# Kernel optimization log

Measured on AMD Instinct MI355X. Metric: run time of the kernel, lower is better.

Reference implementation:

```python
import jax, jax.numpy as jnp
import numpy as np

B, S, D = 2, 2048, 1024
H = 16            # attention heads
KVH = 4           # key/value heads
G = H // KVH      # group_size = 4
HD = D // H       # head_dim = 64
ROPE_THETA = 10000.0


def rope(x):
    # x: [B, S, D]; interleaved-pair rotary embedding over full last dim
    d = x.shape[-1]
    inv_freq = 1.0 / (ROPE_THETA ** (jnp.arange(0, d, 2, dtype=jnp.float32) / d))  # [d/2]
    ang = jnp.arange(x.shape[1], dtype=jnp.float32)[:, None] * inv_freq[None, :]   # [S, d/2]
    cos, sin = jnp.cos(ang), jnp.sin(ang)
    x1, x2 = x[..., 0::2], x[..., 1::2]
    r1 = x1 * cos - x2 * sin
    r2 = x1 * sin + x2 * cos
    out = jnp.stack([r1, r2], axis=-1).reshape(x.shape)
    return out


def setup_inputs() -> dict:
    key = jax.random.key(0)
    kx, kq, kk, kv = jax.random.split(key, 4)
    x = jax.random.normal(kx, (B, S, D), dtype=jnp.float32)
    # mark last 256 positions of batch element 1 as padding via NaN
    x = x.at[1, S - 256:, :].set(jnp.nan)
    scale = 1.0 / np.sqrt(D)
    Wq = jax.random.normal(kq, (D, D), dtype=jnp.float32) * scale
    Wk = jax.random.normal(kk, (D, D // G), dtype=jnp.float32) * scale
    Wv = jax.random.normal(kv, (D, D // G), dtype=jnp.float32) * scale
    return {"x": x, "Wq": Wq, "Wk": Wk, "Wv": Wv}


def reference(x, Wq, Wk, Wv):
    pad = jnp.isnan(x)                      # [B,S,D]
    x = jnp.where(pad, 0.0, x)
    key_pad = jnp.any(pad, axis=-1)         # [B,S] True = padded token

    q = x @ Wq                              # [B,S,D]
    k = jnp.repeat(x @ Wk, G, axis=-1)      # grouped KV, repeat_interleave -> [B,S,D]
    v = jnp.repeat(x @ Wv, G, axis=-1)

    q = rope(q)
    k = rope(k)

    def split_heads(t):
        return t.reshape(B, S, H, HD).transpose(0, 2, 1, 3)  # [B,H,S,HD]

    q, k, v = split_heads(q), split_heads(k), split_heads(v)

    scores = jnp.einsum('bhqd,bhkd->bhqk', q, k) / np.sqrt(HD)
    causal = jnp.tril(jnp.ones((S, S), dtype=bool))
    allow = causal[None, None, :, :] & (~key_pad)[:, None, None, :]
    scores = jnp.where(allow, scores, -1e9)
    attn = jax.nn.softmax(scores, axis=-1)
    out = jnp.einsum('bhqk,bhkd->bhqd', attn, v)
    return out.transpose(0, 2, 1, 3).reshape(B, S, D)
```

## Files before the change

kernel.cpp:

```cpp
#include <hip/hip_runtime.h>
#include <hip/hip_bf16.h>
#include <math.h>

typedef unsigned short u16;
typedef unsigned int u32;
typedef __bf16 bf16x8 __attribute__((ext_vector_type(8)));
typedef float fx4 __attribute__((ext_vector_type(4)));

#define MFMA16(a, b, c) __builtin_amdgcn_mfma_f32_16x16x32_bf16(a, b, c, 0, 0, 0)

static constexpr int Bb = 2, Ss = 2048, Dd = 1024, Hh = 16, DKV = 256;
static constexpr int NQKV = 1536;
static constexpr int ROWS = Bb * Ss;
static constexpr float L2T_OVER = 0.0259525632f;
static constexpr float SC2 = 0.18033688f;
static constexpr int PSTR = 76;

__device__ __forceinline__ u16 f2bf(float f) {
    union { float f; u32 i; } v; v.f = f;
    u32 u = v.i;
    return (u16)((u + 0x7FFFu + ((u >> 16) & 1u)) >> 16);
}
__device__ __forceinline__ u16 bfr(float f) {
    return (u16)((__float_as_uint(f) + 0x8000u) >> 16);
}

__device__ __forceinline__ void gl16(const u16* g, u16* l) {
    __builtin_amdgcn_global_load_lds(
        (const __attribute__((address_space(1))) void*)g,
        (__attribute__((address_space(3))) void*)l, 16, 0, 0);
}

template <int CTRL>
__device__ __forceinline__ float dppf(float x) {
    return __int_as_float(
        __builtin_amdgcn_mov_dpp(__float_as_int(x), CTRL, 0xF, 0xF, true));
}
__device__ __forceinline__ float rsum16(float x) {
    x += dppf<0xB1>(x);
    x += dppf<0x4E>(x);
    x += dppf<0x124>(x);
    x += dppf<0x128>(x);
    return x;
}

__global__ void pre_kernel(const float* __restrict__ x, const float* __restrict__ Wq,
                           const float* __restrict__ Wk, const float* __restrict__ Wv,
                           u16* __restrict__ xc, u32* __restrict__ kpb,
                           u16* __restrict__ wAll) {
    __shared__ u16 tile[32][33];
    __shared__ int flag;
    int bid = blockIdx.x, t = threadIdx.x;
    if (bid < 4096) {
        int row = bid;
        if (t == 0) flag = 0;
        __syncthreads();
        float4 d = *(const float4*)(x + (size_t)row * Dd + t * 4);
        int any = 0;
        float a0 = d.x, a1 = d.y, a2 = d.z, a3 = d.w;
        if ((__float_as_uint(a0) & 0x7FFFFFFFu) > 0x7F800000u) { a0 = 0.f; any = 1; }
        if ((__float_as_uint(a1) & 0x7FFFFFFFu) > 0x7F800000u) { a1 = 0.f; any = 1; }
        if ((__float_as_uint(a2) & 0x7FFFFFFFu) > 0x7F800000u) { a2 = 0.f; any = 1; }
        if ((__float_as_uint(a3) & 0x7FFFFFFFu) > 0x7F800000u) { a3 = 0.f; any = 1; }
        if (any) atomicOr(&flag, 1);
        uint2 o;
        o.x = (u32)f2bf(a0) | ((u32)f2bf(a1) << 16);
        o.y = (u32)f2bf(a2) | ((u32)f2bf(a3) << 16);
        *(uint2*)(xc + (size_t)row * Dd + t * 4) = o;
        __syncthreads();
        if (t == 0 && flag) {
            int b = row >> 11, s = row & (Ss - 1);
            atomicOr(&kpb[b * 64 + (s >> 5)], 1u << (s & 31));
        }
        return;
    }
    const float* in; u16* out; int C, bx, by;
    if (bid < 5120) { int i = bid - 4096; in = Wq; out = wAll; C = Dd; bx = i & 31; by = i >> 5; }
    else if (bid < 5376) { int i = bid - 5120; in = Wk; out = wAll + (size_t)Dd * Dd; C = DKV; bx = i & 7; by = i >> 3; }
    else { int i = bid - 5376; in = Wv; out = wAll + (size_t)1280 * Dd; C = DKV; bx = i & 7; by = i >> 3; }
    int c0 = bx * 32, r0 = by * 32;
    int tx = t & 31, ty = t >> 5;
    for (int i = 0; i < 32; i += 8)
        tile[ty + i][tx] = f2bf(in[(size_t)(r0 + ty + i) * C + c0 + tx]);
    __syncthreads();
    for (int i = 0; i < 32; i += 8)
        out[(size_t)(c0 + ty + i) * Dd + r0 + tx] = tile[tx][ty + i];
}

__global__ __launch_bounds__(256) void gemm_qkv(
    const u16* __restrict__ A, const u16* __restrict__ Bt, u16* __restrict__ C) {
    __shared__ __align__(16) u16 As[2][128 * 32];
    __shared__ __align__(16) u16 Bs[2][128 * 32];
    int t = threadIdx.x, w = t >> 6, lane = t & 63;
    int l15 = lane & 15, quad = lane >> 4;
    int col0 = blockIdx.x * 128, row0 = blockIdx.y * 128;
    int wm = w >> 1, wn = w & 1;
    fx4 acc[4][4];
#pragma unroll
    for (int i = 0; i < 4; ++i)
#pragma unroll
        for (int j = 0; j < 4; ++j) acc[i][j] = (fx4){0.f, 0.f, 0.f, 0.f};

    auto stage = [&](int kb, int buf) {
#pragma unroll
        for (int i = 0; i < 2; ++i) {
            int slot = i * 256 + t;
            int row = slot >> 2, p = slot & 3, g = p ^ ((row >> 1) & 3);
            gl16(A + (size_t)(row0 + row) * Dd + kb * 32 + g * 8,
                 &As[buf][(i * 256 + w * 64) * 8]);
            gl16(Bt + (size_t)(col0 + row) * Dd + kb * 32 + g * 8,
                 &Bs[buf][(i * 256 + w * 64) * 8]);
        }
    };

    stage(0, 0);
    int buf = 0;
    for (int kb = 0; kb < 32; ++kb) {
        __syncthreads();
        if (kb + 1 < 32) stage(kb + 1, buf ^ 1);
        bf16x8 af[4], bfr4[4];
#pragma unroll
        for (int mi = 0; mi < 4; ++mi) {
            int row = wm * 64 + mi * 16 + l15;
            af[mi] = *(const bf16x8*)(&As[buf][row * 32 + ((quad ^ ((row >> 1) & 3)) * 8)]);
        }
#pragma unroll
        for (int ni = 0; ni < 4; ++ni) {
            int row = wn * 64 + ni * 16 + l15;
            bfr4[ni] = *(const bf16x8*)(&Bs[buf][row * 32 + ((quad ^ ((row >> 1) & 3)) * 8)]);
        }
#pragma unroll
        for (int mi = 0; mi < 4; ++mi)
#pragma unroll
            for (int ni = 0; ni < 4; ++ni)
                acc[mi][ni] = MFMA16(af[mi], bfr4[ni], acc[mi][ni]);
        buf ^= 1;
    }
#pragma unroll
    for (int mi = 0; mi < 4; ++mi) {
        int rbase = row0 + wm * 64 + mi * 16 + quad * 4;
#pragma unroll
        for (int ni = 0; ni < 4; ++ni) {
            int ccol = col0 + wn * 64 + ni * 16 + l15;
#pragma unroll
            for (int r = 0; r < 4; ++r)
                C[(size_t)(rbase + r) * NQKV + ccol] = f2bf(acc[mi][ni][r]);
        }
    }
}

__global__ void post_kernel(const u16* __restrict__ qkv, u16* __restrict__ kr,
                            u16* __restrict__ vtb) {
    __shared__ u16 tile[32][33];
    int bid = blockIdx.x, t = threadIdx.x;
    if (bid < 4096) {
        int row = bid;
        float pos = (float)(row & (Ss - 1));
        float kv = __uint_as_float(((u32)qkv[(size_t)row * NQKV + Dd + t]) << 16);
        float j0 = (float)(2 * t), j1 = j0 + 1.0f;
        float f0 = exp2f(-j0 * L2T_OVER), f1 = exp2f(-j1 * L2T_OVER);
        float s0, c0, s1, c1;
        sincosf(pos * f0, &s0, &c0);
        sincosf(pos * f1, &s1, &c1);
        float r0 = kv * (c0 - s0), r1 = kv * (s0 + c0);
        float r2 = kv * (c1 - s1), r3 = kv * (s1 + c1);
        uint2 o;
        o.x = (u32)f2bf(r0) | ((u32)f2bf(r1) << 16);
        o.y = (u32)f2bf(r2) | ((u32)f2bf(r3) << 16);
        *(uint2*)(kr + (size_t)row * Dd + t * 4) = o;
        return;
    }
    int i = bid - 4096;
    int b = i >> 9, by = (i & 511) >> 3, bx = i & 7;
    int c0 = bx * 32, r0 = by * 32;
    int tx = t & 31, ty = t >> 5;
    for (int k = 0; k < 32; k += 8)
        tile[ty + k][tx] = qkv[(size_t)(b * Ss + r0 + ty + k) * NQKV + 1280 + c0 + tx];
    __syncthreads();
    for (int k = 0; k < 32; k += 8)
        vtb[(size_t)(b * DKV + c0 + ty + k) * Ss + r0 + tx] = tile[tx][ty + k];
}

__device__ __forceinline__ bf16x8 ropeFrag(uint4 raw, float pos, float jbase) {
    u32 W[4] = {raw.x, raw.y, raw.z, raw.w};
    union { u32 u[4]; bf16x8 v; } o;
#pragma unroll
    for (int c = 0; c < 4; ++c) {
        float x0 = __uint_as_float(W[c] << 16);
        float x1 = __uint_as_float(W[c] & 0xFFFF0000u);
        float f = exp2f(-(jbase + (float)c) * L2T_OVER);
        float sn, cs;
        sincosf(pos * f, &sn, &cs);
        float r0 = x0 * cs - x1 * sn, r1 = x0 * sn + x1 * cs;
        o.u[c] = (u32)f2bf(r0) | ((u32)f2bf(r1) << 16);
    }
    return o.v;
}

__global__ __launch_bounds__(256) void attn_kernel(
    const u16* __restrict__ qkv, const u16* __restrict__ kr,
    const u16* __restrict__ vt, const u32* __restrict__ kpb,
    float* __restrict__ out) {
    __shared__ __align__(16) u16 Ks[2][64 * 64];
    __shared__ __align__(16) u16 Vs[2][16 * 64];
    __shared__ __align__(16) u16 Ps[4][16 * PSTR];

    int t = threadIdx.x, w = t >> 6, lane = t & 63;
    int l15 = lane & 15, quad = lane >> 4;
    int bid = blockIdx.x;
    int u = bid >> 5, g = u >> 3, i = u & 7;
    int tile = (g == 0) ? (31 - i) : (g == 1) ? (16 + i) : (g == 2) ? (15 - i) : i;
    int hh = bid & 31, b = hh >> 4, h = hh & 15;
    int q0 = tile * 64;
    int nkb = tile + 1;

    int pos = q0 + w * 16 + l15;
    const u16* qp = qkv + (size_t)(b * Ss + pos) * NQKV + h * 64;
    float jb = (float)(h * 32 + quad * 4);
    bf16x8 qf0 = ropeFrag(*(const uint4*)(qp + quad * 8), (float)pos, jb);
    bf16x8 qf1 = ropeFrag(*(const uint4*)(qp + 32 + quad * 8), (float)pos, jb + 16.f);

    auto stageK = [&](int k0, int buf) {
#pragma unroll
        for (int i2 = 0; i2 < 2; ++i2) {
            int row = i2 * 32 + w * 8 + (lane >> 3);
            int gg = (lane & 7) ^ (row & 7);
            gl16(kr + (size_t)(b * Ss + k0 + row) * Dd + h * 64 + gg * 8,
                 &Ks[buf][(i2 * 32 + w * 8) * 64]);
        }
    };
    auto stageV = [&](int k0, int buf) {
        if (w < 2) {
            int row = w * 8 + (lane >> 3);
            int gg = (lane & 7) ^ (row & 7);
            gl16(vt + (size_t)(b * DKV + h * 16 + row) * Ss + k0 + gg * 8,
                 &Vs[buf][(w * 8) * 64]);
        }
    };

    float l_lane[4] = {0.f, 0.f, 0.f, 0.f};
    fx4 oacc = (fx4){0.f, 0.f, 0.f, 0.f};

    stageK(0, 0);
    stageV(0, 0);
    int buf = 0;
    const int qrb = q0 + w * 16 + quad * 4;
    const int qmin = q0 + w * 16;

    for (int kb = 0; kb < nkb; ++kb) {
        int k0 = kb * 64;
        __syncthreads();
        if (kb + 1 < nkb) { stageK(k0 + 64, buf ^ 1); stageV(k0 + 64, buf ^ 1); }

        fx4 s[4];
#pragma unroll
        for (int tt = 0; tt < 4; ++tt) {
            const u16* kb_ = &Ks[buf][(tt * 16 + l15) * 64];
            bf16x8 kf0 = *(const bf16x8*)(kb_ + ((quad ^ (l15 & 7)) * 8));
            bf16x8 kf1 = *(const bf16x8*)(kb_ + (((quad + 4) ^ (l15 & 7)) * 8));
            fx4 z = (fx4){0.f, 0.f, 0.f, 0.f};
            fx4 a = MFMA16(qf0, kf0, z);
            s[tt] = MFMA16(qf1, kf1, a);
        }

        u32 pw0 = kpb[b * 64 + (k0 >> 5)];
        u32 pw1 = kpb[b * 64 + (k0 >> 5) + 1];
        bool fast = (k0 + 63 <= qmin) & ((pw0 | pw1) == 0u);

        float e[4][4];
        if (fast) {
#pragma unroll
            for (int tt = 0; tt < 4; ++tt)
#pragma unroll
                for (int r = 0; r < 4; ++r)
                    e[tt][r] = exp2f(fmaf(s[tt][r], SC2, -32.f));
        } else {
            u32 padb[4];
#pragma unroll
            for (int tt = 0; tt < 4; ++tt)
                padb[tt] = ((tt & 2 ? pw1 : pw0) >> ((tt * 16 + l15) & 31)) & 1u;
#pragma unroll
            for (int r = 0; r < 4; ++r) {
                int qq = qrb + r;
#pragma unroll
                for (int tt = 0; tt < 4; ++tt) {
                    float ee = exp2f(fmaf(s[tt][r], SC2, -32.f));
                    e[tt][r] = (k0 + tt * 16 + l15 <= qq && !padb[tt]) ? ee : 0.f;
                }
            }
        }

#pragma unroll
        for (int r = 0; r < 4; ++r) {
            l_lane[r] += (e[0][r] + e[1][r]) + (e[2][r] + e[3][r]);
            int prow = (quad * 4 + r) * PSTR + l15;
            Ps[w][prow + 0] = bfr(e[0][r]);
            Ps[w][prow + 16] = bfr(e[1][r]);
            Ps[w][prow + 32] = bfr(e[2][r]);
            Ps[w][prow + 48] = bfr(e[3][r]);
        }

#pragma unroll
        for (int hh2 = 0; hh2 < 2; ++hh2) {
            bf16x8 vf = *(const bf16x8*)(&Vs[buf][l15 * 64 + (((quad + 4 * hh2) ^ (l15 & 7)) * 8)]);
            bf16x8 pf = *(const bf16x8*)(&Ps[w][l15 * PSTR + hh2 * 32 + quad * 8]);
            oacc = MFMA16(pf, vf, oacc);
        }
        buf ^= 1;
    }

#pragma unroll
    for (int r = 0; r < 4; ++r) {
        float l_row = rsum16(l_lane[r]);
        float a = oacc[r] / l_row;
        float4 o4 = {a, a, a, a};
        *(float4*)(out + (size_t)(b * Ss + qrb + r) * Dd + h * 64 + l15 * 4) = o4;
    }
}

extern "C" void kernel_launch(void* const* d_in, const int* in_sizes, int n_in,
                              void* d_out, int out_size, void* d_ws, size_t ws_size,
                              hipStream_t stream) {
    const float* x = (const float*)d_in[0];
    const float* Wq = (const float*)d_in[1];
    const float* Wk = (const float*)d_in[2];
    const float* Wv = (const float*)d_in[3];
    float* out = (float*)d_out;

    char* ws = (char*)d_ws;
    const size_t SZ_XC = (size_t)ROWS * Dd * 2;
    const size_t SZ_KPB = 4096;
    const size_t SZ_WALL = (size_t)NQKV * Dd * 2;
    const size_t SZ_QKV = (size_t)ROWS * NQKV * 2;

    size_t off = 0;
    u16* xc = (u16*)(ws + off);
    u16* krope = (u16*)(ws + off); off += SZ_XC;
    u32* kpb = (u32*)(ws + off); off += SZ_KPB;
    u16* wAll = (u16*)(ws + off);
    u16* vtb = (u16*)(ws + off); off += SZ_WALL;
    u16* qkv = (u16*)(ws + off); off += SZ_QKV;
    (void)ws_size; (void)in_sizes; (void)n_in; (void)out_size;

    hipMemsetAsync(kpb, 0, 2 * 64 * 4, stream);
    pre_kernel<<<5632, 256, 0, stream>>>(x, Wq, Wk, Wv, xc, kpb, wAll);
    gemm_qkv<<<dim3(NQKV / 128, ROWS / 128), 256, 0, stream>>>(xc, wAll, qkv);
    post_kernel<<<5120, 256, 0, stream>>>(qkv, krope, vtb);
    attn_kernel<<<1024, 256, 0, stream>>>(qkv, krope, vtb, kpb, out);
}
```

Baseline: 155.3 us.

## Split attention KV range across units with separate reduce, narrow GEMM N-tile

The attention kernel now splits each causal query tile's key range into chunks of up to eight key blocks, launching 2560 blocks instead of 1024 so work is more evenly balanced across CUs. Partial unnormalized outputs and row sums go to workspace, and a new reduce kernel sums them and normalizes. This is sound only because softmax here uses a fixed max and no running max. Separately, the QKV GEMM tile width drops from 128 to 64 columns, doubling its grid for better occupancy. The cost is an extra kernel launch, extra workspace traffic for partials, and less reuse per GEMM block.

Measured after the change: 159.1 us. 1.02x slower.

```diff
diff --git a/kernel.cpp b/kernel.cpp
--- a/kernel.cpp
+++ b/kernel.cpp
@@ -15,6 +15,8 @@
 static constexpr float L2T_OVER = 0.0259525632f;
 static constexpr float SC2 = 0.18033688f;
 static constexpr int PSTR = 76;
+static constexpr int NUNITS = 80;
+static constexpr int NBLK_ATTN = NUNITS * 32;
 
 __device__ __forceinline__ u16 f2bf(float f) {
     union { float f; u32 i; } v; v.f = f;
@@ -90,16 +92,16 @@
 __global__ __launch_bounds__(256) void gemm_qkv(
     const u16* __restrict__ A, const u16* __restrict__ Bt, u16* __restrict__ C) {
     __shared__ __align__(16) u16 As[2][128 * 32];
-    __shared__ __align__(16) u16 Bs[2][128 * 32];
+    __shared__ __align__(16) u16 Bs[2][64 * 32];
     int t = threadIdx.x, w = t >> 6, lane = t & 63;
     int l15 = lane & 15, quad = lane >> 4;
-    int col0 = blockIdx.x * 128, row0 = blockIdx.y * 128;
+    int col0 = blockIdx.x * 64, row0 = blockIdx.y * 128;
     int wm = w >> 1, wn = w & 1;
-    fx4 acc[4][4];
+    fx4 acc[4][2];
 #pragma unroll
     for (int i = 0; i < 4; ++i)
 #pragma unroll
-        for (int j = 0; j < 4; ++j) acc[i][j] = (fx4){0.f, 0.f, 0.f, 0.f};
+        for (int j = 0; j < 2; ++j) acc[i][j] = (fx4){0.f, 0.f, 0.f, 0.f};
 
     auto stage = [&](int kb, int buf) {
 #pragma unroll
@@ -108,8 +110,11 @@
             int row = slot >> 2, p = slot & 3, g = p ^ ((row >> 1) & 3);
             gl16(A + (size_t)(row0 + row) * Dd + kb * 32 + g * 8,
                  &As[buf][(i * 256 + w * 64) * 8]);
+        }
+        {
+            int row = t >> 2, p = t & 3, g = p ^ ((row >> 1) & 3);
             gl16(Bt + (size_t)(col0 + row) * Dd + kb * 32 + g * 8,
-                 &Bs[buf][(i * 256 + w * 64) * 8]);
+                 &Bs[buf][(w * 64) * 8]);
         }
     };
 
@@ -118,30 +123,30 @@
     for (int kb = 0; kb < 32; ++kb) {
         __syncthreads();
         if (kb + 1 < 32) stage(kb + 1, buf ^ 1);
-        bf16x8 af[4], bfr4[4];
+        bf16x8 af[4], bfr2[2];
 #pragma unroll
         for (int mi = 0; mi < 4; ++mi) {
             int row = wm * 64 + mi * 16 + l15;
             af[mi] = *(const bf16x8*)(&As[buf][row * 32 + ((quad ^ ((row >> 1) & 3)) * 8)]);
         }
 #pragma unroll
-        for (int ni = 0; ni < 4; ++ni) {
-            int row = wn * 64 + ni * 16 + l15;
-            bfr4[ni] = *(const bf16x8*)(&Bs[buf][row * 32 + ((quad ^ ((row >> 1) & 3)) * 8)]);
+        for (int ni = 0; ni < 2; ++ni) {
+            int row = wn * 32 + ni * 16 + l15;
+            bfr2[ni] = *(const bf16x8*)(&Bs[buf][row * 32 + ((quad ^ ((row >> 1) & 3)) * 8)]);
         }
 #pragma unroll
         for (int mi = 0; mi < 4; ++mi)
 #pragma unroll
-            for (int ni = 0; ni < 4; ++ni)
-                acc[mi][ni] = MFMA16(af[mi], bfr4[ni], acc[mi][ni]);
+            for (int ni = 0; ni < 2; ++ni)
+                acc[mi][ni] = MFMA16(af[mi], bfr2[ni], acc[mi][ni]);
         buf ^= 1;
     }
 #pragma unroll
     for (int mi = 0; mi < 4; ++mi) {
         int rbase = row0 + wm * 64 + mi * 16 + quad * 4;
 #pragma unroll
-        for (int ni = 0; ni < 4; ++ni) {
-            int ccol = col0 + wn * 64 + ni * 16 + l15;
+        for (int ni = 0; ni < 2; ++ni) {
+            int ccol = col0 + wn * 32 + ni * 16 + l15;
 #pragma unroll
             for (int r = 0; r < 4; ++r)
                 C[(size_t)(rbase + r) * NQKV + ccol] = f2bf(acc[mi][ni][r]);
@@ -200,7 +205,7 @@
 __global__ __launch_bounds__(256) void attn_kernel(
     const u16* __restrict__ qkv, const u16* __restrict__ kr,
     const u16* __restrict__ vt, const u32* __restrict__ kpb,
-    float* __restrict__ out) {
+    float* __restrict__ po, float* __restrict__ pl) {
     __shared__ __align__(16) u16 Ks[2][64 * 64];
     __shared__ __align__(16) u16 Vs[2][16 * 64];
     __shared__ __align__(16) u16 Ps[4][16 * PSTR];
@@ -208,11 +213,16 @@
     int t = threadIdx.x, w = t >> 6, lane = t & 63;
     int l15 = lane & 15, quad = lane >> 4;
     int bid = blockIdx.x;
-    int u = bid >> 5, g = u >> 3, i = u & 7;
-    int tile = (g == 0) ? (31 - i) : (g == 1) ? (16 + i) : (g == 2) ? (15 - i) : i;
-    int hh = bid & 31, b = hh >> 4, h = hh & 15;
+    int col = bid & 31, b = col >> 4, h = col & 15;
+    int ub = (NUNITS - 1) - (bid >> 5);
+    int tile, unit;
+    if (ub < 8) { tile = ub; unit = 0; }
+    else if (ub < 24) { int v = ub - 8; tile = 8 + (v >> 1); unit = v & 1; }
+    else if (ub < 48) { int v = ub - 24; int d3 = v / 3; tile = 16 + d3; unit = v - 3 * d3; }
+    else { int v = ub - 48; tile = 24 + (v >> 2); unit = v & 3; }
     int q0 = tile * 64;
-    int nkb = tile + 1;
+    int kbStart = unit * 8;
+    int kbEnd = min(kbStart + 8, tile + 1);
 
     int pos = q0 + w * 16 + l15;
     const u16* qp = qkv + (size_t)(b * Ss + pos) * NQKV + h * 64;
@@ -241,16 +251,16 @@
     float l_lane[4] = {0.f, 0.f, 0.f, 0.f};
     fx4 oacc = (fx4){0.f, 0.f, 0.f, 0.f};
 
-    stageK(0, 0);
-    stageV(0, 0);
+    stageK(kbStart * 64, 0);
+    stageV(kbStart * 64, 0);
     int buf = 0;
     const int qrb = q0 + w * 16 + quad * 4;
     const int qmin = q0 + w * 16;
 
-    for (int kb = 0; kb < nkb; ++kb) {
+    for (int kb = kbStart; kb < kbEnd; ++kb) {
         int k0 = kb * 64;
         __syncthreads();
-        if (kb + 1 < nkb) { stageK(k0 + 64, buf ^ 1); stageV(k0 + 64, buf ^ 1); }
+        if (kb + 1 < kbEnd) { stageK(k0 + 64, buf ^ 1); stageV(k0 + 64, buf ^ 1); }
 
         fx4 s[4];
 #pragma unroll
@@ -311,10 +321,41 @@
 
 #pragma unroll
     for (int r = 0; r < 4; ++r) {
+        int qrow = w * 16 + quad * 4 + r;
+        po[(size_t)bid * 1024 + qrow * 16 + l15] = oacc[r];
         float l_row = rsum16(l_lane[r]);
-        float a = oacc[r] / l_row;
-        float4 o4 = {a, a, a, a};
-        *(float4*)(out + (size_t)(b * Ss + qrb + r) * Dd + h * 64 + l15 * 4) = o4;
+        if (l15 == 0) pl[bid * 64 + qrow] = l_row;
+    }
+}
+
+__global__ __launch_bounds__(256) void reduce_kernel(
+    const float* __restrict__ po, const float* __restrict__ pl,
+    float* __restrict__ out) {
+    int rbid = blockIdx.x;
+    int col = rbid & 31, tile = rbid >> 5;
+    int b = col >> 4, h = col & 15;
+    int base, n;
+    if (tile < 8) { base = tile; n = 1; }
+    else if (tile < 16) { base = 8 + (tile - 8) * 2; n = 2; }
+    else if (tile < 24) { base = 24 + (tile - 16) * 3; n = 3; }
+    else { base = 48 + (tile - 24) * 4; n = 4; }
+    int t = threadIdx.x;
+    int q = t >> 2, ug = (t & 3) * 4;
+    float l = 0.f;
+    fx4 o = (fx4){0.f, 0.f, 0.f, 0.f};
+    for (int j = 0; j < n; ++j) {
+        int slot = ((NUNITS - 1) - (base + j)) * 32 + col;
+        l += pl[slot * 64 + q];
+        fx4 v = *(const fx4*)(po + (size_t)slot * 1024 + q * 16 + ug);
+        o += v;
+    }
+    float inv = 1.0f / l;
+    size_t ob = (size_t)(b * Ss + tile * 64 + q) * Dd + h * 64 + ug * 4;
+#pragma unroll
+    for (int j = 0; j < 4; ++j) {
+        float val = o[j] * inv;
+        float4 o4 = {val, val, val, val};
+        *(float4*)(out + ob + j * 4) = o4;
     }
 }
 
@@ -332,6 +373,8 @@
     const size_t SZ_KPB = 4096;
     const size_t SZ_WALL = (size_t)NQKV * Dd * 2;
     const size_t SZ_QKV = (size_t)ROWS * NQKV * 2;
+    const size_t SZ_PO = (size_t)NBLK_ATTN * 1024 * 4;
+    const size_t SZ_PL = (size_t)NBLK_ATTN * 64 * 4;
 
     size_t off = 0;
     u16* xc = (u16*)(ws + off);
@@ -340,11 +383,14 @@
     u16* wAll = (u16*)(ws + off);
     u16* vtb = (u16*)(ws + off); off += SZ_WALL;
     u16* qkv = (u16*)(ws + off); off += SZ_QKV;
+    float* po = (float*)(ws + off); off += SZ_PO;
+    float* pl = (float*)(ws + off); off += SZ_PL;
     (void)ws_size; (void)in_sizes; (void)n_in; (void)out_size;
 
     hipMemsetAsync(kpb, 0, 2 * 64 * 4, stream);
     pre_kernel<<<5632, 256, 0, stream>>>(x, Wq, Wk, Wv, xc, kpb, wAll);
-    gemm_qkv<<<dim3(NQKV / 128, ROWS / 128), 256, 0, stream>>>(xc, wAll, qkv);
+    gemm_qkv<<<dim3(NQKV / 64, ROWS / 128), 256, 0, stream>>>(xc, wAll, qkv);
     post_kernel<<<5120, 256, 0, stream>>>(qkv, krope, vtb);
-    attn_kernel<<<1024, 256, 0, stream>>>(qkv, krope, vtb, kpb, out);
-}
+    attn_kernel<<<NBLK_ATTN, 256, 0, stream>>>(qkv, krope, vtb, kpb, po, pl);
+    reduce_kernel<<<1024, 256, 0, stream>>>(po, pl, out);
+}
```
